# Kernel optimization log

Measured on AMD Instinct MI355X. Metric: run time of the kernel, lower is better.

## Reference

```python
import jax, jax.numpy as jnp
import numpy as np

K = 3   # num nearest neighbors (init k)
P = 2   # IDW power (init p)


def setup_inputs() -> dict:
    key = jax.random.key(0)
    k1, k2, k3, k4 = jax.random.split(key, 4)
    B, N, M, C = 8, 16384, 1024, 256
    xyz = jax.random.normal(k1, (B, N, 3), dtype=jnp.float32)
    sampled_xyz = jax.random.normal(k2, (B, M, 3), dtype=jnp.float32)
    sampled_features = jax.random.normal(k3, (B, M, C), dtype=jnp.float32)
    masks = jax.random.randint(k4, (B, N), 0, 2, dtype=jnp.int32)
    return {"xyz": xyz, "sampled_xyz": sampled_xyz,
            "sampled_features": sampled_features, "masks": masks}


def reference(xyz, sampled_xyz, sampled_features, masks):
    # xyz: [B,N,3], sampled_xyz: [B,M,3], sampled_features: [B,M,C], masks: [B,N]
    # Squared pairwise distances [B,N,M] (same math as the chunked torch loop).
    delta = xyz[:, :, None, :] - sampled_xyz[:, None, :, :]
    dists = jnp.sum(delta * delta, axis=-1)
    # k smallest distances -> negate and take top-k.
    neg_top, idx = jax.lax.top_k(-dists, K)          # [B,N,K]
    min_dists = jnp.maximum(-neg_top, 1e-10)
    weights = 1.0 / (min_dists ** P + 1e-10)
    weights = weights / jnp.sum(weights, axis=-1, keepdims=True)
    # Gather neighbor features: [B,N,K,C]
    gathered = jax.vmap(lambda f, i: f[i])(sampled_features, idx)
    interpolated = jnp.sum(gathered * weights[..., None], axis=2)  # [B,N,C]
    # Invalid (masked-out) rows stay zero, matching the padded scatter.
    valid = (masks != 0).astype(interpolated.dtype)
    return interpolated * valid[..., None]
```

## Files before the change

### kernel.cpp

```cpp
#include <hip/hip_runtime.h>

constexpr int B = 8;
constexpr int N = 16384;
constexpr int M = 1024;
constexpr int C = 256;
constexpr int PTS = 64;
constexpr int QW  = 4;

typedef float vf16 __attribute__((ext_vector_type(16)));

__global__ __launch_bounds__(256, 8) void upsample_idw_kernel(
    const float* __restrict__ xyz,
    const float* __restrict__ sxyz,
    const float* __restrict__ feats,
    const int*   __restrict__ masks,
    float*       __restrict__ out)
{
    const int tid = threadIdx.x;
    const int w   = tid >> 6;
    const int l   = tid & 63;
    const int blk = blockIdx.x;
    const int b     = blk & 7;
    const int nbase = (blk >> 3) << 6;

    __shared__ unsigned long long s_key[PTS][QW][3];
    __shared__ float s_w[PTS][3];
    __shared__ int   s_j[PTS][4];

    const float* xp = xyz + ((size_t)b * N + nbase + l) * 3;
    const float x = xp[0], y = xp[1], z = xp[2];

    const float* bbase = sxyz + (size_t)b * (M * 3);
    const int qoff = __builtin_amdgcn_readfirstlane((tid >> 6) * (256 * 12));

    float d0 = __builtin_inff(), d1 = __builtin_inff(), d2 = __builtin_inff();
    int   i0 = 0, i1 = 0, i2 = 0;

    for (int ch = 0; ch < 16; ++ch) {
        vf16 ca, cb, cc;
        const int off = qoff + ch * 192;
        asm volatile(
            "s_load_dwordx16 %0, %3, %4\n\t"
            "s_load_dwordx16 %1, %3, %4 offset:64\n\t"
            "s_load_dwordx16 %2, %3, %4 offset:128\n\t"
            "s_waitcnt lgkmcnt(0)"
            : "=&s"(ca), "=&s"(cb), "=&s"(cc)
            : "s"(bbase), "s"(off));
        #pragma unroll
        for (int j = 0; j < 16; ++j) {
            const int f0 = 3 * j, f1 = 3 * j + 1, f2 = 3 * j + 2;
            const float cx = (f0 < 16) ? ca[f0 & 15] : (f0 < 32) ? cb[f0 & 15] : cc[f0 & 15];
            const float cy = (f1 < 16) ? ca[f1 & 15] : (f1 < 32) ? cb[f1 & 15] : cc[f1 & 15];
            const float cz = (f2 < 16) ? ca[f2 & 15] : (f2 < 32) ? cb[f2 & 15] : cc[f2 & 15];
            const float dx = __fsub_rn(cx, x);
            const float dy = __fsub_rn(cy, y);
            const float dz = __fsub_rn(cz, z);
            const float d  = __fadd_rn(__fadd_rn(__fmul_rn(dx, dx), __fmul_rn(dy, dy)),
                                       __fmul_rn(dz, dz));
            if (__ballot(d < d2) != 0ULL) {
                const int m = ch * 16 + j;
                const bool lt0 = d < d0, lt1 = d < d1, lt2 = d < d2;
                i2 = lt1 ? i1 : (lt2 ? m : i2);
                i1 = lt0 ? i0 : (lt1 ? m : i1);
                i0 = lt0 ? m  : i0;
                const float nd2 = __builtin_amdgcn_fmed3f(d1, d2, d);
                const float nd1 = __builtin_amdgcn_fmed3f(d0, d1, d);
                d2 = nd2; d1 = nd1; d0 = fminf(d0, d);
            }
        }
    }

    const unsigned base = (unsigned)(w * 256);
    s_key[l][w][0] = ((unsigned long long)__float_as_uint(d0) << 32) | (base + (unsigned)i0);
    s_key[l][w][1] = ((unsigned long long)__float_as_uint(d1) << 32) | (base + (unsigned)i1);
    s_key[l][w][2] = ((unsigned long long)__float_as_uint(d2) << 32) | (base + (unsigned)i2);
    __syncthreads();

    if (tid < PTS) {
        unsigned long long k0 = ~0ULL, k1 = ~0ULL, k2 = ~0ULL;
        #pragma unroll
        for (int q = 0; q < QW; ++q) {
            #pragma unroll
            for (int s = 0; s < 3; ++s) {
                const unsigned long long k = s_key[tid][q][s];
                const bool lt0 = k < k0, lt1 = k < k1, lt2 = k < k2;
                k2 = lt1 ? k1 : (lt2 ? k : k2);
                k1 = lt0 ? k0 : (lt1 ? k : k1);
                k0 = lt0 ? k  : k0;
            }
        }
        const float e0 = __uint_as_float((unsigned)(k0 >> 32));
        const float e1 = __uint_as_float((unsigned)(k1 >> 32));
        const float e2 = __uint_as_float((unsigned)(k2 >> 32));
        const float m0 = fmaxf(e0, 1e-10f);
        const float m1 = fmaxf(e1, 1e-10f);
        const float m2 = fmaxf(e2, 1e-10f);
        float w0 = 1.0f / (m0 * m0 + 1e-10f);
        float w1 = 1.0f / (m1 * m1 + 1e-10f);
        float w2 = 1.0f / (m2 * m2 + 1e-10f);
        const int valid = masks[(size_t)b * N + nbase + tid];
        const float scale = valid ? (1.0f / (w0 + w1 + w2)) : 0.0f;
        s_w[tid][0] = w0 * scale;
        s_w[tid][1] = w1 * scale;
        s_w[tid][2] = w2 * scale;
        s_j[tid][0] = (int)(unsigned)k0;
        s_j[tid][1] = (int)(unsigned)k1;
        s_j[tid][2] = (int)(unsigned)k2;
        s_j[tid][3] = valid;
    }
    __syncthreads();

    const int pq = tid >> 6;
    const int cq = tid & 63;
    const float4* Fb4 = (const float4*)(feats + (size_t)b * (M * C));
    float4* op4 = (float4*)(out + (((size_t)b * N + nbase) * C));

    for (int p0 = 0; p0 < PTS; p0 += 4) {
        const int p = p0 + pq;
        const int vld = __builtin_amdgcn_readfirstlane(s_j[p][3]);
        float4 acc = make_float4(0.f, 0.f, 0.f, 0.f);
        if (vld) {
            const int j0 = __builtin_amdgcn_readfirstlane(s_j[p][0]);
            const int j1 = __builtin_amdgcn_readfirstlane(s_j[p][1]);
            const int j2 = __builtin_amdgcn_readfirstlane(s_j[p][2]);
            const float w0 = __uint_as_float(
                __builtin_amdgcn_readfirstlane((int)__float_as_uint(s_w[p][0])));
            const float w1 = __uint_as_float(
                __builtin_amdgcn_readfirstlane((int)__float_as_uint(s_w[p][1])));
            const float w2 = __uint_as_float(
                __builtin_amdgcn_readfirstlane((int)__float_as_uint(s_w[p][2])));
            const float4 f0 = Fb4[j0 * 64 + cq];
            const float4 f1 = Fb4[j1 * 64 + cq];
            const float4 f2 = Fb4[j2 * 64 + cq];
            acc.x = fmaf(w2, f2.x, fmaf(w1, f1.x, w0 * f0.x));
            acc.y = fmaf(w2, f2.y, fmaf(w1, f1.y, w0 * f0.y));
            acc.z = fmaf(w2, f2.z, fmaf(w1, f1.z, w0 * f0.z));
            acc.w = fmaf(w2, f2.w, fmaf(w1, f1.w, w0 * f0.w));
        }
        op4[p * 64 + cq] = acc;
    }
}

extern "C" void kernel_launch(void* const* d_in, const int* in_sizes, int n_in,
                              void* d_out, int out_size, void* d_ws, size_t ws_size,
                              hipStream_t stream) {
    const float* xyz   = (const float*)d_in[0];
    const float* sxyz  = (const float*)d_in[1];
    const float* feats = (const float*)d_in[2];
    const int*   masks = (const int*)d_in[3];
    float*       out   = (float*)d_out;

    dim3 grid(B * N / PTS);
    dim3 block(256);
    hipLaunchKernelGGL(upsample_idw_kernel, grid, block, 0, stream,
                       xyz, sxyz, feats, masks, out);
}
```

Baseline: 66.62 us.

## Warp-specialize scan and gather waves with double-buffered LDS handoff

Each block now handles four tiles of 64 points with 512 threads. Four waves compute KNN distances and four consumer waves merge top-3, compute weights and gather features. The two groups hand off through double-buffered shared keys and atomic counters, so the memory-bound gather overlaps the compute-bound scan. The ballot early-skip in the inner loop is removed. This adds spin-wait overhead, cuts the grid by a factor of four, and the consumer waves idle while the first tile is scanned.

```diff
diff --git a/kernel.cpp b/kernel.cpp
--- a/kernel.cpp
+++ b/kernel.cpp
@@ -4,12 +4,12 @@
 constexpr int N = 16384;
 constexpr int M = 1024;
 constexpr int C = 256;
-constexpr int PTS = 64;
-constexpr int QW  = 4;
+constexpr int PTS   = 64;
+constexpr int TILES = 4;
 
 typedef float vf16 __attribute__((ext_vector_type(16)));
 
-__global__ __launch_bounds__(256, 8) void upsample_idw_kernel(
+__global__ __launch_bounds__(512, 4) void upsample_idw_kernel(
     const float* __restrict__ xyz,
     const float* __restrict__ sxyz,
     const float* __restrict__ feats,
@@ -21,123 +21,136 @@
     const int l   = tid & 63;
     const int blk = blockIdx.x;
     const int b     = blk & 7;
-    const int nbase = (blk >> 3) << 6;
+    const int pbase = (blk >> 3) * (TILES * PTS);
 
-    __shared__ unsigned long long s_key[PTS][QW][3];
-    __shared__ float s_w[PTS][3];
-    __shared__ int   s_j[PTS][4];
+    __shared__ unsigned long long s_key[2][PTS][4][3];
+    __shared__ int s_scan_cnt[2];
+    __shared__ int s_write_cnt[2];
 
-    const float* xp = xyz + ((size_t)b * N + nbase + l) * 3;
-    const float x = xp[0], y = xp[1], z = xp[2];
+    if (tid < 2) { s_scan_cnt[tid] = 0; s_write_cnt[tid] = 0; }
+    __syncthreads();
 
     const float* bbase = sxyz + (size_t)b * (M * 3);
-    const int qoff = __builtin_amdgcn_readfirstlane((tid >> 6) * (256 * 12));
 
-    float d0 = __builtin_inff(), d1 = __builtin_inff(), d2 = __builtin_inff();
-    int   i0 = 0, i1 = 0, i2 = 0;
+    if (w < 4) {
+        const int q = w;
+        const int qoff = __builtin_amdgcn_readfirstlane(q * (256 * 12));
 
-    for (int ch = 0; ch < 16; ++ch) {
-        vf16 ca, cb, cc;
-        const int off = qoff + ch * 192;
-        asm volatile(
-            "s_load_dwordx16 %0, %3, %4\n\t"
-            "s_load_dwordx16 %1, %3, %4 offset:64\n\t"
-            "s_load_dwordx16 %2, %3, %4 offset:128\n\t"
-            "s_waitcnt lgkmcnt(0)"
-            : "=&s"(ca), "=&s"(cb), "=&s"(cc)
-            : "s"(bbase), "s"(off));
-        #pragma unroll
-        for (int j = 0; j < 16; ++j) {
-            const int f0 = 3 * j, f1 = 3 * j + 1, f2 = 3 * j + 2;
-            const float cx = (f0 < 16) ? ca[f0 & 15] : (f0 < 32) ? cb[f0 & 15] : cc[f0 & 15];
-            const float cy = (f1 < 16) ? ca[f1 & 15] : (f1 < 32) ? cb[f1 & 15] : cc[f1 & 15];
-            const float cz = (f2 < 16) ? ca[f2 & 15] : (f2 < 32) ? cb[f2 & 15] : cc[f2 & 15];
-            const float dx = __fsub_rn(cx, x);
-            const float dy = __fsub_rn(cy, y);
-            const float dz = __fsub_rn(cz, z);
-            const float d  = __fadd_rn(__fadd_rn(__fmul_rn(dx, dx), __fmul_rn(dy, dy)),
-                                       __fmul_rn(dz, dz));
-            if (__ballot(d < d2) != 0ULL) {
-                const int m = ch * 16 + j;
-                const bool lt0 = d < d0, lt1 = d < d1, lt2 = d < d2;
-                i2 = lt1 ? i1 : (lt2 ? m : i2);
-                i1 = lt0 ? i0 : (lt1 ? m : i1);
-                i0 = lt0 ? m  : i0;
-                const float nd2 = __builtin_amdgcn_fmed3f(d1, d2, d);
-                const float nd1 = __builtin_amdgcn_fmed3f(d0, d1, d);
-                d2 = nd2; d1 = nd1; d0 = fminf(d0, d);
+        for (int t = 0; t < TILES; ++t) {
+            const int buf = t & 1, k = t >> 1;
+            if (k > 0) {
+                while (__hip_atomic_load(&s_write_cnt[buf], __ATOMIC_ACQUIRE,
+                                         __HIP_MEMORY_SCOPE_WORKGROUP) < 4 * k)
+                    __builtin_amdgcn_s_sleep(1);
             }
+
+            const int pt = pbase + t * PTS + l;
+            const float* xp = xyz + ((size_t)b * N + pt) * 3;
+            const float x = xp[0], y = xp[1], z = xp[2];
+
+            float d0 = __builtin_inff(), d1 = __builtin_inff(), d2 = __builtin_inff();
+            int   i0 = 0, i1 = 0, i2 = 0;
+
+            for (int ch = 0; ch < 16; ++ch) {
+                vf16 ca, cb, cc;
+                const int off = qoff + ch * 192;
+                asm volatile(
+                    "s_load_dwordx16 %0, %3, %4\n\t"
+                    "s_load_dwordx16 %1, %3, %4 offset:64\n\t"
+                    "s_load_dwordx16 %2, %3, %4 offset:128\n\t"
+                    "s_waitcnt lgkmcnt(0)"
+                    : "=&s"(ca), "=&s"(cb), "=&s"(cc)
+                    : "s"(bbase), "s"(off));
+                #pragma unroll
+                for (int j = 0; j < 16; ++j) {
+                    const int f0 = 3 * j, f1 = 3 * j + 1, f2 = 3 * j + 2;
+                    const float cx = (f0 < 16) ? ca[f0 & 15] : (f0 < 32) ? cb[f0 & 15] : cc[f0 & 15];
+                    const float cy = (f1 < 16) ? ca[f1 & 15] : (f1 < 32) ? cb[f1 & 15] : cc[f1 & 15];
+                    const float cz = (f2 < 16) ? ca[f2 & 15] : (f2 < 32) ? cb[f2 & 15] : cc[f2 & 15];
+                    const float dx = __fsub_rn(cx, x);
+                    const float dy = __fsub_rn(cy, y);
+                    const float dz = __fsub_rn(cz, z);
+                    const float d  = __fadd_rn(__fadd_rn(__fmul_rn(dx, dx), __fmul_rn(dy, dy)),
+                                               __fmul_rn(dz, dz));
+                    const int m = ch * 16 + j;
+                    const bool lt0 = d < d0, lt1 = d < d1, lt2 = d < d2;
+                    i2 = lt1 ? i1 : (lt2 ? m : i2);
+                    i1 = lt0 ? i0 : (lt1 ? m : i1);
+                    i0 = lt0 ? m  : i0;
+                    const float nd2 = __builtin_amdgcn_fmed3f(d1, d2, d);
+                    const float nd1 = __builtin_amdgcn_fmed3f(d0, d1, d);
+                    d2 = nd2; d1 = nd1; d0 = fminf(d0, d);
+                }
+            }
+
+            const unsigned base = (unsigned)(q * 256);
+            s_key[buf][l][q][0] = ((unsigned long long)__float_as_uint(d0) << 32) | (base + (unsigned)i0);
+            s_key[buf][l][q][1] = ((unsigned long long)__float_as_uint(d1) << 32) | (base + (unsigned)i1);
+            s_key[buf][l][q][2] = ((unsigned long long)__float_as_uint(d2) << 32) | (base + (unsigned)i2);
+
+            if (l == 0)
+                __hip_atomic_fetch_add(&s_scan_cnt[buf], 1, __ATOMIC_RELEASE,
+                                       __HIP_MEMORY_SCOPE_WORKGROUP);
         }
-    }
+    } else {
+        const int wv = w - 4;
+        const float4* Fb4 = (const float4*)(feats + (size_t)b * (M * C));
 
-    const unsigned base = (unsigned)(w * 256);
-    s_key[l][w][0] = ((unsigned long long)__float_as_uint(d0) << 32) | (base + (unsigned)i0);
-    s_key[l][w][1] = ((unsigned long long)__float_as_uint(d1) << 32) | (base + (unsigned)i1);
-    s_key[l][w][2] = ((unsigned long long)__float_as_uint(d2) << 32) | (base + (unsigned)i2);
-    __syncthreads();
+        for (int t = 0; t < TILES; ++t) {
+            const int buf = t & 1, k = t >> 1;
+            while (__hip_atomic_load(&s_scan_cnt[buf], __ATOMIC_ACQUIRE,
+                                     __HIP_MEMORY_SCOPE_WORKGROUP) < 4 * (k + 1))
+                __builtin_amdgcn_s_sleep(1);
 
-    if (tid < PTS) {
-        unsigned long long k0 = ~0ULL, k1 = ~0ULL, k2 = ~0ULL;
-        #pragma unroll
-        for (int q = 0; q < QW; ++q) {
-            #pragma unroll
-            for (int s = 0; s < 3; ++s) {
-                const unsigned long long k = s_key[tid][q][s];
-                const bool lt0 = k < k0, lt1 = k < k1, lt2 = k < k2;
-                k2 = lt1 ? k1 : (lt2 ? k : k2);
-                k1 = lt0 ? k0 : (lt1 ? k : k1);
-                k0 = lt0 ? k  : k0;
+            float4* op4 = (float4*)(out + ((size_t)b * N + pbase + t * PTS) * C);
+
+            for (int i = 0; i < 16; ++i) {
+                const int p = 4 * i + wv;
+                unsigned long long k0 = ~0ULL, k1 = ~0ULL, k2 = ~0ULL;
+                #pragma unroll
+                for (int q = 0; q < 4; ++q) {
+                    #pragma unroll
+                    for (int s = 0; s < 3; ++s) {
+                        const unsigned long long kk = s_key[buf][p][q][s];
+                        const bool lt0 = kk < k0, lt1 = kk < k1, lt2 = kk < k2;
+                        k2 = lt1 ? k1 : (lt2 ? kk : k2);
+                        k1 = lt0 ? k0 : (lt1 ? kk : k1);
+                        k0 = lt0 ? kk : k0;
+                    }
+                }
+                const float e0 = __uint_as_float((unsigned)(k0 >> 32));
+                const float e1 = __uint_as_float((unsigned)(k1 >> 32));
+                const float e2 = __uint_as_float((unsigned)(k2 >> 32));
+                const float m0 = fmaxf(e0, 1e-10f);
+                const float m1 = fmaxf(e1, 1e-10f);
+                const float m2 = fmaxf(e2, 1e-10f);
+                float w0 = 1.0f / (m0 * m0 + 1e-10f);
+                float w1 = 1.0f / (m1 * m1 + 1e-10f);
+                float w2 = 1.0f / (m2 * m2 + 1e-10f);
+                const int valid = masks[(size_t)b * N + pbase + t * PTS + p];
+                const float scale = valid ? (1.0f / (w0 + w1 + w2)) : 0.0f;
+                w0 *= scale; w1 *= scale; w2 *= scale;
+
+                float4 acc = make_float4(0.f, 0.f, 0.f, 0.f);
+                if (valid) {
+                    const int j0 = (int)(unsigned)k0;
+                    const int j1 = (int)(unsigned)k1;
+                    const int j2 = (int)(unsigned)k2;
+                    const float4 f0 = Fb4[j0 * 64 + l];
+                    const float4 f1 = Fb4[j1 * 64 + l];
+                    const float4 f2 = Fb4[j2 * 64 + l];
+                    acc.x = fmaf(w2, f2.x, fmaf(w1, f1.x, w0 * f0.x));
+                    acc.y = fmaf(w2, f2.y, fmaf(w1, f1.y, w0 * f0.y));
+                    acc.z = fmaf(w2, f2.z, fmaf(w1, f1.z, w0 * f0.z));
+                    acc.w = fmaf(w2, f2.w, fmaf(w1, f1.w, w0 * f0.w));
+                }
+                op4[p * 64 + l] = acc;
             }
+
+            if (l == 0)
+                __hip_atomic_fetch_add(&s_write_cnt[buf], 1, __ATOMIC_RELEASE,
+                                       __HIP_MEMORY_SCOPE_WORKGROUP);
         }
-        const float e0 = __uint_as_float((unsigned)(k0 >> 32));
-        const float e1 = __uint_as_float((unsigned)(k1 >> 32));
-        const float e2 = __uint_as_float((unsigned)(k2 >> 32));
-        const float m0 = fmaxf(e0, 1e-10f);
-        const float m1 = fmaxf(e1, 1e-10f);
-        const float m2 = fmaxf(e2, 1e-10f);
-        float w0 = 1.0f / (m0 * m0 + 1e-10f);
-        float w1 = 1.0f / (m1 * m1 + 1e-10f);
-        float w2 = 1.0f / (m2 * m2 + 1e-10f);
-        const int valid = masks[(size_t)b * N + nbase + tid];
-        const float scale = valid ? (1.0f / (w0 + w1 + w2)) : 0.0f;
-        s_w[tid][0] = w0 * scale;
-        s_w[tid][1] = w1 * scale;
-        s_w[tid][2] = w2 * scale;
-        s_j[tid][0] = (int)(unsigned)k0;
-        s_j[tid][1] = (int)(unsigned)k1;
-        s_j[tid][2] = (int)(unsigned)k2;
-        s_j[tid][3] = valid;
-    }
-    __syncthreads();
-
-    const int pq = tid >> 6;
-    const int cq = tid & 63;
-    const float4* Fb4 = (const float4*)(feats + (size_t)b * (M * C));
-    float4* op4 = (float4*)(out + (((size_t)b * N + nbase) * C));
-
-    for (int p0 = 0; p0 < PTS; p0 += 4) {
-        const int p = p0 + pq;
-        const int vld = __builtin_amdgcn_readfirstlane(s_j[p][3]);
-        float4 acc = make_float4(0.f, 0.f, 0.f, 0.f);
-        if (vld) {
-            const int j0 = __builtin_amdgcn_readfirstlane(s_j[p][0]);
-            const int j1 = __builtin_amdgcn_readfirstlane(s_j[p][1]);
-            const int j2 = __builtin_amdgcn_readfirstlane(s_j[p][2]);
-            const float w0 = __uint_as_float(
-                __builtin_amdgcn_readfirstlane((int)__float_as_uint(s_w[p][0])));
-            const float w1 = __uint_as_float(
-                __builtin_amdgcn_readfirstlane((int)__float_as_uint(s_w[p][1])));
-            const float w2 = __uint_as_float(
-                __builtin_amdgcn_readfirstlane((int)__float_as_uint(s_w[p][2])));
-            const float4 f0 = Fb4[j0 * 64 + cq];
-            const float4 f1 = Fb4[j1 * 64 + cq];
-            const float4 f2 = Fb4[j2 * 64 + cq];
-            acc.x = fmaf(w2, f2.x, fmaf(w1, f1.x, w0 * f0.x));
-            acc.y = fmaf(w2, f2.y, fmaf(w1, f1.y, w0 * f0.y));
-            acc.z = fmaf(w2, f2.z, fmaf(w1, f1.z, w0 * f0.z));
-            acc.w = fmaf(w2, f2.w, fmaf(w1, f1.w, w0 * f0.w));
-        }
-        op4[p * 64 + cq] = acc;
     }
 }
 
@@ -150,8 +163,8 @@
     const int*   masks = (const int*)d_in[3];
     float*       out   = (float*)d_out;
 
-    dim3 grid(B * N / PTS);
-    dim3 block(256);
+    dim3 grid(B * N / (TILES * PTS));
+    dim3 block(512);
     hipLaunchKernelGGL(upsample_idw_kernel, grid, block, 0, stream,
                        xyz, sxyz, feats, masks, out);
 }
```

Result: slower. 94.28 us (+41.5%).
